# Optimization experiments

Measured on AMD Instinct MI355X. Metric: run time of the kernel, lower is better.

The kernel has to match this reference:

```python
import jax, jax.numpy as jnp
import numpy as np

N_EXPERTS = 16
NUM_SHARDS = 1
CAPACITY_FACTOR = 1.25
EPS = 0.01


def setup_inputs() -> dict:
    key = jax.random.key(0)
    k1, k2, k3 = jax.random.split(key, 3)
    C, T, D = 4, 4096, 1024
    E = N_EXPERTS * NUM_SHARDS
    inputs = jax.random.normal(k1, (C, T, D), dtype=jnp.float32)
    # trunc-normal router weight, std = (initializer_factor / ((D + E)/2))**0.5
    std = (1.0 / ((D + E) / 2.0)) ** 0.5
    router_weight = jax.random.truncated_normal(k2, -2.0, 2.0, (E, D), dtype=jnp.float32) * std
    # multiplicative jitter in [1-eps, 1+eps)
    noise = (1.0 - EPS) + 2.0 * EPS * jax.random.uniform(k3, (C, T, D), dtype=jnp.float32)
    return {"inputs": inputs, "router_weight": router_weight, "noise": noise}


def reference(inputs, router_weight, noise):
    C, T, D = inputs.shape
    E = N_EXPERTS * NUM_SHARDS
    expert_capacity = max(int(CAPACITY_FACTOR * T // N_EXPERTS), 1)

    x = inputs.astype(jnp.float32) * noise                      # gate inputs with jitter
    router_logits = jnp.einsum('ctd,ed->cte', x, router_weight)  # [C,T,E]
    router_probs = jax.nn.softmax(router_logits, axis=-1)
    expert_gate = jnp.max(router_probs, axis=-1)                 # [C,T]
    expert_index = jnp.argmax(router_probs, axis=-1)             # [C,T] int

    expert_mask = jax.nn.one_hot(expert_index, E, dtype=jnp.float32)  # [C,T,E]

    # load-balancing aux loss (before capacity truncation)
    density1 = expert_mask.mean(axis=1)          # [C,E]
    density1_proxy = router_probs.mean(axis=1)   # [C,E]
    aux_loss = (density1 * density1_proxy).sum() * E

    # capacity-limited position tracking
    position_in_expert = jnp.cumsum(expert_mask, axis=1) * expert_mask            # [C,T,E]
    expert_mask = expert_mask * (position_in_expert.astype(jnp.int32) < expert_capacity)
    expert_mask_flat = expert_mask.sum(axis=-1)                                    # [C,T]
    position_in_expert = (jnp.cumsum(expert_mask, axis=1) * expert_mask).astype(jnp.int32)
    expert_gate = expert_gate * expert_mask_flat

    # Faithful replication of torch scatter_(dim=1) on a [C,T,E,1] tensor with
    # index shape [C,T,1,1]: only the (e=0, cap=0) slice is written, at token
    # position == expert_index[c,t].
    c_idx = jnp.arange(C)[:, None]
    expert_index_inf = jnp.zeros((C, T, E, 1), jnp.float32).at[c_idx, expert_index, 0, 0].set(1.0)

    # one-hot over capacity slot (scatter along dim 3)
    position_inf = jax.nn.one_hot(position_in_expert, expert_capacity, dtype=jnp.float32)  # [C,T,E,cap]

    combine_tensor = (expert_gate[:, :, None, None]
                      * expert_mask_flat[:, :, None, None]
                      * expert_index_inf
                      * position_inf)
    dispatch_tensor = combine_tensor.astype(bool)
    return dispatch_tensor, combine_tensor, aux_loss
```

## Files before the change

### kernel.cpp

```cpp
#include <hip/hip_runtime.h>
#include <math.h>

#define C_DIM 4
#define T_DIM 4096
#define D_DIM 1024
#define E_DIM 16
#define CAP   320
#define CT    (C_DIM * T_DIM)
#define OUT_ONE ((size_t)CT * E_DIM * CAP)

#define NBLOCKS 1024
#define N4      ((2 * OUT_ONE) / 4)
#define F4_PER_BLOCK (N4 / NBLOCKS)

__host__ __device__ constexpr int bitrev6(int i) {
    return ((i & 1) << 5) | ((i & 2) << 3) | ((i & 4) << 1)
         | ((i & 8) >> 1) | ((i & 16) >> 3) | ((i & 32) >> 5);
}


__global__ void fused_router_fill_kernel(
    const float* __restrict__ in, const float* __restrict__ w,
    const float* __restrict__ noise, float* __restrict__ gate,
    int* __restrict__ index, float* __restrict__ auxpart,
    int* __restrict__ counts, float4* __restrict__ out4)
{
    __shared__ float psum[E_DIM];
    __shared__ int   hcnt[E_DIM];
    const int tid = threadIdx.x;
    if (tid < E_DIM) { psum[tid] = 0.0f; hcnt[tid] = 0; }
    __syncthreads();

    const int wave = tid >> 6;
    const int lane = tid & 63;
    const int g0   = blockIdx.x * 16 + wave * 4;

    const float4 z = make_float4(0.f, 0.f, 0.f, 0.f);
    float4* dst = out4 + (size_t)blockIdx.x * F4_PER_BLOCK;

    if (blockIdx.x & 1) {
        #pragma unroll 8
        for (int i = tid; i < F4_PER_BLOCK; i += 256)
            dst[i] = z;
    }

    float val[64];
    #pragma unroll
    for (int i = 0; i < 64; ++i) val[i] = 0.0f;

    #pragma unroll 1
    for (int r = 0; r < 4; ++r) {
        const int d0 = r * 256 + lane * 4;
        float4 x[4];
        #pragma unroll
        for (int tk = 0; tk < 4; ++tk) {
            const float4 a = *(const float4*)(in    + (size_t)(g0 + tk) * D_DIM + d0);
            const float4 n = *(const float4*)(noise + (size_t)(g0 + tk) * D_DIM + d0);
            x[tk] = make_float4(a.x * n.x, a.y * n.y, a.z * n.z, a.w * n.w);
        }
        #pragma unroll
        for (int e = 0; e < 16; ++e) {
            const float4 wv = *(const float4*)(w + e * D_DIM + d0);
            #pragma unroll
            for (int tk = 0; tk < 4; ++tk) {
                val[bitrev6(tk * 16 + e)] += x[tk].x * wv.x + x[tk].y * wv.y
                                           + x[tk].z * wv.z + x[tk].w * wv.w;
            }
        }
    }

    #pragma unroll
    for (int m = 0; m < 6; ++m) {
        const int half = 32 >> m;
        const int bit  = (lane >> m) & 1;
        #pragma unroll
        for (int j = 0; j < half; ++j) {
            const float send = bit ? val[j] : val[j + half];
            const float recv = __shfl_xor(send, 1 << m, 64);
            val[j] = (bit ? val[j + half] : val[j]) + recv;
        }
    }

    const int tk = lane >> 4;
    const int e  = lane & 15;
    const float logit = val[0];
    const int g = g0 + tk;

    float mv = logit; int am = e;
    #pragma unroll
    for (int msk = 1; msk <= 8; msk <<= 1) {
        const float ov = __shfl_xor(mv, msk, 64);
        const int   oe = __shfl_xor(am, msk, 64);
        if (ov > mv || (ov == mv && oe < am)) { mv = ov; am = oe; }
    }

    const float p = __expf(logit - mv);
    float s = p;
    #pragma unroll
    for (int msk = 1; msk <= 8; msk <<= 1)
        s += __shfl_xor(s, msk, 64);

    const float inv = 1.0f / s;
    if (e == am) {
        gate[g]  = inv;
        index[g] = am;
        atomicAdd(&hcnt[am], 1);
    }

    float pn = p * inv;
    pn += __shfl_xor(pn, 16, 64);
    pn += __shfl_xor(pn, 32, 64);
    if (lane < 16)
        atomicAdd(&psum[e], pn);

    __syncthreads();
    if (tid < 16) {
        const int c = blockIdx.x >> 8;
        atomicAdd(&auxpart[c * 16 + tid], psum[tid]);
        atomicAdd(&counts [c * 16 + tid], hcnt[tid]);
    }

    if (!(blockIdx.x & 1)) {
        #pragma unroll 8
        for (int i = tid; i < F4_PER_BLOCK; i += 256)
            dst[i] = z;
    }
}

__global__ __launch_bounds__(64) void finalize_kernel(
    const float* __restrict__ gate, const int* __restrict__ index,
    const int* __restrict__ counts, const float* __restrict__ auxpart,
    float* __restrict__ out)
{
    const int id = threadIdx.x;
    const int c  = id >> 4;
    const int tp = id & 15;
    const int cnt = counts[id];

    float term = ((float)cnt * (1.0f / T_DIM)) * (auxpart[id] * (1.0f / T_DIM));

    if (cnt > 0) {
        const int g     = c * T_DIM + tp;
        const int myidx = index[g];
        int s = 0;
        if (myidx == 0) {
            int r = 0;
            for (int t = 0; t <= tp; ++t)
                r += (index[c * T_DIM + t] == 0);
            s = r;
        }
        const size_t off = ((size_t)g * E_DIM + 0) * CAP + (size_t)s;
        out[off]            = 1.0f;
        out[OUT_ONE + off]  = gate[g];
    }

    #pragma unroll
    for (int off = 32; off; off >>= 1)
        term += __shfl_down(term, off, 64);
    if (id == 0)
        out[2 * OUT_ONE] = 16.0f * term;
}

extern "C" void kernel_launch(void* const* d_in, const int* in_sizes, int n_in,
                              void* d_out, int out_size, void* d_ws, size_t ws_size,
                              hipStream_t stream) {
    const float* in    = (const float*)d_in[0];
    const float* w     = (const float*)d_in[1];
    const float* noise = (const float*)d_in[2];
    float* out = (float*)d_out;

    char* ws = (char*)d_ws;
    float* auxpart = (float*)(ws);
    int*   counts  = (int*)(ws + 256);
    float* gate    = (float*)(ws + 512);
    int*   index   = (int*)(ws + 512 + 65536);

    (void)hipMemsetAsync(ws, 0, 512, stream);

    fused_router_fill_kernel<<<dim3(NBLOCKS), dim3(256), 0, stream>>>(
        in, w, noise, gate, index, auxpart, counts, (float4*)out);
    finalize_kernel<<<dim3(1), dim3(64), 0, stream>>>(gate, index, counts, auxpart, out);
}
```

Measured before the change: 179.5 us.

## Double-buffer router input loads through LDS with async global_load_lds

Replaces direct per-chunk global loads of inputs and noise with asynchronous global-to-LDS copies into a per-wave double buffer, using explicit waitcnt to overlap the next chunk's loads with the current chunk's dot products. It aims to hide global memory latency in the router GEMV. It adds 64KB of LDS per block, which may reduce occupancy and the overlap of the zero-fill stores. It also relies on hand-counted vmcnt ordering.

```diff
diff --git a/kernel.cpp b/kernel.cpp
--- a/kernel.cpp
+++ b/kernel.cpp
@@ -19,12 +19,54 @@
 }
 
 
+__device__ __forceinline__ void gl_lds16(const float* g, float* l) {
+    __builtin_amdgcn_global_load_lds(
+        (const __attribute__((address_space(1))) void*)g,
+        (__attribute__((address_space(3))) void*)l,
+        16, 0, 0);
+}
+
+__device__ __forceinline__ void stage_chunk(
+    const float* __restrict__ in, const float* __restrict__ noise,
+    float (*buf)[256], int g0, int r, int lane)
+{
+    const size_t base = (size_t)g0 * D_DIM + r * 256 + lane * 4;
+    #pragma unroll
+    for (int j = 0; j < 4; ++j)
+        gl_lds16(in + base + (size_t)j * D_DIM, &buf[j][0]);
+    #pragma unroll
+    for (int j = 0; j < 4; ++j)
+        gl_lds16(noise + base + (size_t)j * D_DIM, &buf[4 + j][0]);
+}
+
+__device__ __forceinline__ void compute_chunk(
+    const float* __restrict__ w, float (*buf)[256], float* val, int r, int lane)
+{
+    const int d0 = r * 256 + lane * 4;
+    float4 x[4];
+    #pragma unroll
+    for (int tk = 0; tk < 4; ++tk) {
+        const float4 a = *(const float4*)&buf[tk][lane * 4];
+        const float4 n = *(const float4*)&buf[4 + tk][lane * 4];
+        x[tk] = make_float4(a.x * n.x, a.y * n.y, a.z * n.z, a.w * n.w);
+    }
+    #pragma unroll
+    for (int e = 0; e < 16; ++e) {
+        const float4 wv4 = *(const float4*)(w + e * D_DIM + d0);
+        #pragma unroll
+        for (int tk = 0; tk < 4; ++tk)
+            val[bitrev6(tk * 16 + e)] += x[tk].x * wv4.x + x[tk].y * wv4.y
+                                       + x[tk].z * wv4.z + x[tk].w * wv4.w;
+    }
+}
+
 __global__ void fused_router_fill_kernel(
     const float* __restrict__ in, const float* __restrict__ w,
     const float* __restrict__ noise, float* __restrict__ gate,
     int* __restrict__ index, float* __restrict__ auxpart,
     int* __restrict__ counts, float4* __restrict__ out4)
 {
+    __shared__ float stage_lds[4][2][8][256];
     __shared__ float psum[E_DIM];
     __shared__ int   hcnt[E_DIM];
     const int tid = threadIdx.x;
@@ -48,26 +90,27 @@
     #pragma unroll
     for (int i = 0; i < 64; ++i) val[i] = 0.0f;
 
-    #pragma unroll 1
-    for (int r = 0; r < 4; ++r) {
-        const int d0 = r * 256 + lane * 4;
-        float4 x[4];
-        #pragma unroll
-        for (int tk = 0; tk < 4; ++tk) {
-            const float4 a = *(const float4*)(in    + (size_t)(g0 + tk) * D_DIM + d0);
-            const float4 n = *(const float4*)(noise + (size_t)(g0 + tk) * D_DIM + d0);
-            x[tk] = make_float4(a.x * n.x, a.y * n.y, a.z * n.z, a.w * n.w);
-        }
-        #pragma unroll
-        for (int e = 0; e < 16; ++e) {
-            const float4 wv = *(const float4*)(w + e * D_DIM + d0);
-            #pragma unroll
-            for (int tk = 0; tk < 4; ++tk) {
-                val[bitrev6(tk * 16 + e)] += x[tk].x * wv.x + x[tk].y * wv.y
-                                           + x[tk].z * wv.z + x[tk].w * wv.w;
-            }
-        }
-    }
+    float (*sbuf0)[256] = stage_lds[wave][0];
+    float (*sbuf1)[256] = stage_lds[wave][1];
+
+    stage_chunk(in, noise, sbuf0, g0, 0, lane);
+    stage_chunk(in, noise, sbuf1, g0, 1, lane);
+
+    asm volatile("s_waitcnt vmcnt(8)" ::: "memory");
+    compute_chunk(w, sbuf0, val, 0, lane);
+    asm volatile("s_waitcnt lgkmcnt(0)" ::: "memory");
+    stage_chunk(in, noise, sbuf0, g0, 2, lane);
+
+    asm volatile("s_waitcnt vmcnt(8)" ::: "memory");
+    compute_chunk(w, sbuf1, val, 1, lane);
+    asm volatile("s_waitcnt lgkmcnt(0)" ::: "memory");
+    stage_chunk(in, noise, sbuf1, g0, 3, lane);
+
+    asm volatile("s_waitcnt vmcnt(8)" ::: "memory");
+    compute_chunk(w, sbuf0, val, 2, lane);
+
+    asm volatile("s_waitcnt vmcnt(0)" ::: "memory");
+    compute_chunk(w, sbuf1, val, 3, lane);
 
     #pragma unroll
     for (int m = 0; m < 6; ++m) {
```

After: 441.7 us. 2.46x slower.
